# Optimization experiments

Hardware: AMD Instinct MI355X
Metric: run time of the kernel (lower is better)

## Reference

```python
import jax, jax.numpy as jnp
import numpy as np

U, B, S, R = 64, 256, 256, 512
N = 4096
EMA_DECAY = 0.99


def setup_inputs() -> dict:
    key = jax.random.key(0)
    ks = jax.random.split(key, 9)
    q_u = jax.random.uniform(ks[0], (N, U), dtype=jnp.float32)
    q_b = jax.random.uniform(ks[1], (N, B), dtype=jnp.float32)
    q_sigma = jax.random.normal(ks[2], (N, S), dtype=jnp.float32)
    delta_rule_target = jax.random.normal(ks[3], (N, R), dtype=jnp.float32)
    write_mask = jax.random.randint(ks[4], (N,), 0, 2).astype(bool)
    delta_rule_proto = 0.02 * jax.random.normal(ks[5], (U, B, R), dtype=jnp.float32)
    signature_proto = 0.02 * jax.random.normal(ks[6], (U, B, S), dtype=jnp.float32)
    ema_conf = jax.random.uniform(ks[7], (U, B), dtype=jnp.float32)
    usage_count = jnp.maximum(jax.random.uniform(ks[8], (U, B)) - 0.5, 0.0) * 100.0
    return {"q_u": q_u, "q_b": q_b, "q_sigma": q_sigma,
            "delta_rule_target": delta_rule_target, "write_mask": write_mask,
            "delta_rule_proto": delta_rule_proto, "signature_proto": signature_proto,
            "ema_conf": ema_conf, "usage_count": usage_count}


def _l2norm(x):
    return x / jnp.maximum(jnp.linalg.norm(x, axis=-1, keepdims=True), 1e-12)


def reference(q_u, q_b, q_sigma, delta_rule_target, write_mask,
              delta_rule_proto, signature_proto, ema_conf, usage_count):
    # ---------------- retrieve ----------------
    # joint attention over (operator, binding) cells; temperature == 1.0 branch
    joint = q_u[:, :, None] * q_b[:, None, :]                  # [N, U, B]
    valid = (usage_count > 0).astype(joint.dtype)              # [U, B]
    w = joint * valid
    denom = w.sum(axis=(-2, -1), keepdims=True)
    w = jnp.where(denom > 0, w / jnp.maximum(denom, 1e-6), jnp.zeros_like(w))
    memory_delta_rule = jnp.einsum('nub,ubr->nr', w, delta_rule_proto)
    memory_signature = jnp.einsum('nub,ubs->ns', w, signature_proto)
    base_conf = jnp.einsum('nub,ub->n', w, ema_conf)[:, None]  # [N, 1]
    cos = jnp.sum(_l2norm(q_sigma) * _l2norm(memory_signature + 1e-6),
                  axis=-1, keepdims=True)
    signature_agreement = 0.5 * (1.0 + cos)
    memory_conf = jnp.clip(base_conf * signature_agreement, 0.0, 1.0)

    # ---------------- update (vectorized scatter EMA) ----------------
    m = write_mask.astype(q_u.dtype)                           # [N]
    op_conf = q_u.max(axis=-1)
    op_id = jnp.argmax(q_u, axis=-1)
    bind_conf = q_b.max(axis=-1)
    bind_id = jnp.argmax(q_b, axis=-1)
    write_conf = op_conf * bind_conf                           # [N]
    cell = op_id * B + bind_id                                 # [N]
    num_cells = U * B
    wgt = write_conf * m
    sum_w = jax.ops.segment_sum(wgt, cell, num_segments=num_cells)          # [UB]
    sum_d = jax.ops.segment_sum(delta_rule_target * wgt[:, None], cell,
                                num_segments=num_cells)                     # [UB, R]
    sum_s = jax.ops.segment_sum(q_sigma * wgt[:, None], cell,
                                num_segments=num_cells)                     # [UB, S]
    cnt = jax.ops.segment_sum(m, cell, num_segments=num_cells)              # [UB]
    conf_sum = jnp.maximum(sum_w, 1e-6)
    delta_mean = (sum_d / conf_sum[:, None]).reshape(U, B, R)
    sigma_mean = (sum_s / conf_sum[:, None]).reshape(U, B, S)
    conf_mean = (sum_w / jnp.maximum(cnt, 1.0)).reshape(U, B)
    upd = (cnt > 0).reshape(U, B)
    new_delta_proto = jnp.where(upd[:, :, None],
                                EMA_DECAY * delta_rule_proto + (1.0 - EMA_DECAY) * delta_mean,
                                delta_rule_proto)
    new_signature_proto = jnp.where(upd[:, :, None],
                                    EMA_DECAY * signature_proto + (1.0 - EMA_DECAY) * sigma_mean,
                                    signature_proto)
    new_ema_conf = jnp.where(upd,
                             EMA_DECAY * ema_conf + (1.0 - EMA_DECAY) * conf_mean,
                             ema_conf)
    new_usage = usage_count + cnt.reshape(U, B)

    # ---------------- usage stats ----------------
    write_rate = m.mean()
    usage_fraction = (new_usage > 0).astype(jnp.float32).mean()
    dist = new_usage.reshape(-1)
    dist = dist / jnp.maximum(dist.sum(), 1e-6)
    usage_entropy = -(dist * jnp.log(dist + 1e-6)).sum() / np.log(max(2, num_cells))

    return (memory_delta_rule, memory_signature, memory_conf,
            new_delta_proto, new_signature_proto, new_ema_conf, new_usage,
            write_rate, usage_fraction, usage_entropy)
```

## Files before the change

kernel.cpp:

```cpp
#include <hip/hip_runtime.h>
#include <hip/hip_fp8.h>
#include <math.h>

#define NR 4096
#define UD 64
#define BD 256
#define SD 256
#define RD 512
#define UBD 16384
#define DECAY 0.99f

typedef unsigned char u8;
typedef __attribute__((ext_vector_type(4))) float f32x4;
typedef __attribute__((ext_vector_type(2))) long longx2;

#define OFF_MDR   0ull
#define OFF_MSIG  2097152ull
#define OFF_MCONF 3145728ull
#define OFF_NDP   3149824ull
#define OFF_NSP   11538432ull
#define OFF_NEC   15732736ull
#define OFF_NUS   15749120ull
#define OFF_SCAL  15765504ull

static __device__ __forceinline__ u8 f2e4m3(float x) {
  __hip_fp8_e4m3 h(x);
  return (u8)h.__x;
}

static __device__ __forceinline__ void gll16(const void* g, void* l) {
  __builtin_amdgcn_global_load_lds(
      (const __attribute__((address_space(1))) unsigned int*)g,
      (__attribute__((address_space(3))) unsigned int*)l, 16, 0, 0);
}

static __device__ __forceinline__ int perm64(int x) {
  return (((x >> 3) & 3) << 4) | (((x >> 5) & 1) << 3) | (x & 7);
}

__global__ __launch_bounds__(256) void prep_all_kernel(
    const float* __restrict__ q_u, const float* __restrict__ q_b,
    const float* __restrict__ q_sigma_unused,
    const float* __restrict__ dproto, const float* __restrict__ sproto,
    const float* __restrict__ usage, const float* __restrict__ ema,
    const unsigned char* __restrict__ wm,
    u8* __restrict__ qb8, float* __restrict__ quT, u8* __restrict__ PT8,
    float* __restrict__ denom, float* __restrict__ base_raw,
    float* __restrict__ wgt, int* __restrict__ cellid, float* __restrict__ mrow,
    float* __restrict__ sum_w, float* __restrict__ cnt)
{
  __shared__ __attribute__((aligned(16))) u8 sbuf[53248];
  __shared__ int s_flag;
  const int b = blockIdx.x;
  const int tid = threadIdx.x;

  if (b < 1024) {
    const int i = b * 256 + tid;
    const int idx = i * 4;
    const int row = idx >> 8;
    const int bb  = idx & 255;
    const float4 v = *(const float4*)(q_b + (size_t)idx);
    u8 tmp[4] = { f2e4m3(v.x), f2e4m3(v.y), f2e4m3(v.z), f2e4m3(v.w) };
    unsigned int wv; __builtin_memcpy(&wv, tmp, 4);
    const int nb = (bb & ~63) | perm64(bb & 63);
    *(unsigned int*)(qb8 + (size_t)row * BD + nb) = wv;
    return;
  }
  if (b < 1088) {
    float (*s)[65] = (float(*)[65])sbuf;
    const int n0 = (b - 1024) * 64;
    #pragma unroll
    for (int i = 0; i < 16; ++i) {
      const int idx = tid + i * 256;
      const int r = idx >> 6, u = idx & 63;
      s[r][u] = q_u[(size_t)(n0 + r) * UD + u];
    }
    __syncthreads();
    #pragma unroll
    for (int i = 0; i < 16; ++i) {
      const int idx = tid + i * 256;
      const int u = idx >> 6, r = idx & 63;
      quT[(size_t)u * NR + n0 + r] = s[r][u];
    }
    return;
  }
  if (b < 4160) {
    u8 (*s)[68] = (u8(*)[68])sbuf;
    const int idx = b - 1088;
    const int k0 = (idx & 255) * 64;
    const int rblk = idx >> 8;
    const float* src; int ld; int c0s;
    if (rblk < 8) { src = dproto; ld = RD; c0s = rblk * 64; }
    else          { src = sproto; ld = SD; c0s = (rblk - 8) * 64; }
    const int kl = tid >> 4;
    const int rl = (tid & 15) * 4;
    #pragma unroll
    for (int i = 0; i < 4; ++i) {
      const int k = kl + i * 16;
      const bool valid = usage[k0 + k] > 0.f;
      const float4 v = *(const float4*)(src + (size_t)(k0 + k) * ld + c0s + rl);
      s[k][rl + 0] = valid ? f2e4m3(v.x) : (u8)0;
      s[k][rl + 1] = valid ? f2e4m3(v.y) : (u8)0;
      s[k][rl + 2] = valid ? f2e4m3(v.z) : (u8)0;
      s[k][rl + 3] = valid ? f2e4m3(v.w) : (u8)0;
    }
    __syncthreads();
    const int rl2 = tid >> 4;
    const int kl2 = (tid & 15) * 4;
    #pragma unroll
    for (int i = 0; i < 4; ++i) {
      const int r = rl2 + i * 16;
      u8 tmp[4] = { s[kl2 + 0][r], s[kl2 + 1][r], s[kl2 + 2][r], s[kl2 + 3][r] };
      unsigned int wv; __builtin_memcpy(&wv, tmp, 4);
      *(unsigned int*)(PT8 + (size_t)(rblk * 64 + r) * UBD + k0 + perm64(kl2)) = wv;
    }
    return;
  }
  {
    float (*s_qu)[64]   = (float(*)[64])sbuf;
    float (*s_qbv)[256] = (float(*)[256])(sbuf + 4096);
    float (*s_pd)[256]  = (float(*)[256])(sbuf + 20480);
    float (*s_pc)[256]  = (float(*)[256])(sbuf + 36864);
    const int r0 = (b - 4160) * 16;
    {
      const float4 v = *(const float4*)(q_u + (size_t)r0 * UD + tid * 4);
      float* dst = &s_qu[0][0] + tid * 4;
      dst[0] = v.x; dst[1] = v.y; dst[2] = v.z; dst[3] = v.w;
    }
    {
      const float4* src = (const float4*)(q_b + (size_t)r0 * BD);
      float4* dst = (float4*)&s_qbv[0][0];
      #pragma unroll
      for (int i = 0; i < 4; ++i) dst[tid + i * 256] = src[tid + i * 256];
    }
    if (tid == 0) {
      const int*   wi = (const int*)wm;
      const float* wf = (const float*)wm;
      bool is_i32 = true, is_f32 = true;
      #pragma unroll
      for (int i = 0; i < 16; ++i) {
        int v = wi[i];
        if (v != 0 && v != 1) is_i32 = false;
        float f = wf[i];
        if (f != 0.f && f != 1.f) is_f32 = false;
      }
      s_flag = is_i32 ? 2 : (is_f32 ? 1 : 0);
    }
    __syncthreads();
    float accd[16], accc[16];
    #pragma unroll
    for (int r = 0; r < 16; ++r) { accd[r] = 0.f; accc[r] = 0.f; }
    #pragma unroll 2
    for (int u = 0; u < UD; ++u) {
      const float us = usage[u * BD + tid];
      const float em = ema[u * BD + tid];
      const float vm = (us > 0.f) ? 1.f : 0.f;
      const float ev = em * vm;
      #pragma unroll
      for (int r = 0; r < 16; ++r) {
        accd[r] += s_qu[r][u] * vm;
        accc[r] += s_qu[r][u] * ev;
      }
    }
    #pragma unroll
    for (int r = 0; r < 16; ++r) {
      s_pd[r][tid] = accd[r] * s_qbv[r][tid];
      s_pc[r][tid] = accc[r] * s_qbv[r][tid];
    }
    __syncthreads();
    const int w = tid >> 6, l = tid & 63;
    #pragma unroll
    for (int rr = 0; rr < 4; ++rr) {
      const int row = w * 4 + rr;
      float dsum = s_pd[row][l] + s_pd[row][l + 64] + s_pd[row][l + 128] + s_pd[row][l + 192];
      float csum = s_pc[row][l] + s_pc[row][l + 64] + s_pc[row][l + 128] + s_pc[row][l + 192];
      #pragma unroll
      for (int m = 1; m < 64; m <<= 1) {
        dsum += __shfl_xor(dsum, m);
        csum += __shfl_xor(csum, m);
      }
      float bv_ = s_qbv[row][l]; int bi_ = l;
      #pragma unroll
      for (int k = 1; k < 4; ++k) {
        const float v2 = s_qbv[row][l + k * 64];
        if (v2 > bv_) { bv_ = v2; bi_ = l + k * 64; }
      }
      #pragma unroll
      for (int m = 1; m < 64; m <<= 1) {
        const float ov = __shfl_xor(bv_, m);
        const int   oi = __shfl_xor(bi_, m);
        if (ov > bv_ || (ov == bv_ && oi < bi_)) { bv_ = ov; bi_ = oi; }
      }
      float uv_ = s_qu[row][l]; int ui_ = l;
      #pragma unroll
      for (int m = 1; m < 64; m <<= 1) {
        const float ov = __shfl_xor(uv_, m);
        const int   oi = __shfl_xor(ui_, m);
        if (ov > uv_ || (ov == uv_ && oi < ui_)) { uv_ = ov; ui_ = oi; }
      }
      if (l == 0) {
        const int n = r0 + row;
        const int fm = s_flag;
        float m;
        if (fm == 2)      m = (((const int*)wm)[n]   != 0)   ? 1.f : 0.f;
        else if (fm == 1) m = (((const float*)wm)[n] != 0.f) ? 1.f : 0.f;
        else              m = (wm[n] != 0)   ? 1.f : 0.f;
        const float wv = uv_ * bv_ * m;
        const int cell = ui_ * BD + bi_;
        denom[n]    = dsum;
        base_raw[n] = csum;
        wgt[n]      = wv;
        cellid[n]   = cell;
        mrow[n]     = m;
        if (m != 0.f) {
          atomicAdd(&sum_w[cell], wv);
          atomicAdd(&cnt[cell], 1.f);
        }
      }
    }
  }
}

__global__ __launch_bounds__(256, 2) void mfma_gemm_kernel(
    const float* __restrict__ quT, const u8* __restrict__ qb8,
    const u8* __restrict__ PT8, float* __restrict__ out,
    int* __restrict__ tk, int* __restrict__ gf, int* __restrict__ claimed)
{
  __shared__ __attribute__((aligned(16))) u8 smB[4 * 2 * 4096];
  __shared__ __attribute__((aligned(16))) float squT[16 * 128];
  __shared__ int s_work;
  const int tid = threadIdx.x;
  const int wid = tid >> 6, lane = tid & 63;

  const int wr = (wid >> 1) * 64, wc = (wid & 1) * 64;
  const int fr = lane & 15, kg = lane >> 4;
  const int srow  = lane >> 2;
  const int sslot = (lane & 3) ^ ((srow >> 1) & 3);
  u8* myB = smB + wid * 8192;
  int boff[4];
  #pragma unroll
  for (int nn = 0; nn < 4; ++nn)
    boff[nn] = (nn * 16 + fr) * 64 + ((kg ^ ((fr >> 1) & 3)) << 4);

  for (;;) {
    if (tid == 0) {
      unsigned int xcc;
      asm volatile("s_getreg_b32 %0, hwreg(HW_REG_XCC_ID)" : "=s"(xcc));
      const int x = (int)(xcc & 7u);
      const int t = atomicAdd(&tk[x], 1);
      int w = -1;
      if (t < 96) {
        const int cand = x * 96 + t;
        if (atomicCAS(&claimed[cand], 0, 1) == 0) w = cand;
      }
      while (w < 0) {
        const int g = atomicAdd(gf, 1);
        if (g >= 768) { w = -2; break; }
        if (atomicCAS(&claimed[g], 0, 1) == 0) w = g;
      }
      s_work = w;
    }
    __syncthreads();
    const int w = s_work;
    if (w < 0) return;

    const int bx = w & 31;
    const int combo = w >> 5;
    const int by = combo >> 2;
    const int bz = combo & 3;
    const int n0 = bx * 128;
    const int kbeg = bz * (UBD / 4);
    const int ubase = bz * 16;
    const int c0 = by * 128;

    float* obase; int ldO; int cc0;
    if (by < 4) { obase = out + OFF_MDR;  ldO = RD; cc0 = by * 128; }
    else        { obase = out + OFF_MSIG; ldO = SD; cc0 = (by - 4) * 128; }

    longx2 afrag[4][4];
    {
      const u8* ga = qb8 + (size_t)(n0 + wr + fr) * BD + kg * 16;
      #pragma unroll
      for (int m = 0; m < 4; ++m)
        #pragma unroll
        for (int q = 0; q < 4; ++q)
          afrag[m][q] = *(const longx2*)(ga + (size_t)m * 16 * BD + q * 64);
    }

    #pragma unroll
    for (int i = 0; i < 2; ++i) {
      const int u = wid * 4 + i * 2 + (lane >> 5);
      const float* src = quT + (size_t)(ubase + u) * NR + n0 + (lane & 31) * 4;
      gll16(src, (u8*)squT + (wid * 4 + i * 2) * 512);
    }
    const u8* gB = PT8 + (size_t)(c0 + wc + srow) * UBD + kbeg + sslot * 16;
    #pragma unroll
    for (int c = 0; c < 2; ++c)
      #pragma unroll
      for (int j = 0; j < 4; ++j)
        gll16(gB + (size_t)(j * 16) * UBD + c * 64, myB + c * 4096 + j * 1024);
    __syncthreads();

    f32x4 accm[4][4], accu[4][4];
    #pragma unroll
    for (int m = 0; m < 4; ++m)
      #pragma unroll
      for (int nn = 0; nn < 4; ++nn)
        accm[m][nn] = (f32x4){0.f, 0.f, 0.f, 0.f};

    for (int uc = 0; uc < 16; ++uc) {
      #pragma unroll
      for (int p4 = 0; p4 < 4; ++p4) {
        const int ph = uc * 4 + p4;
        if (p4 == 3 && uc == 15) asm volatile("s_waitcnt vmcnt(0)" ::: "memory");
        else                     asm volatile("s_waitcnt vmcnt(4)" ::: "memory");
        const u8* sb = myB + (ph & 1) * 4096;
        longx2 bv[4];
        #pragma unroll
        for (int nn = 0; nn < 4; ++nn)
          bv[nn] = *(const longx2*)(sb + boff[nn]);
        asm volatile("s_waitcnt lgkmcnt(0)" ::: "memory");
        if (!(uc == 15 && p4 >= 2)) {
          const u8* gs = gB + (size_t)(ph + 2) * 64;
          #pragma unroll
          for (int j = 0; j < 4; ++j)
            gll16(gs + (size_t)(j * 16) * UBD, myB + (ph & 1) * 4096 + j * 1024);
        }
        #pragma unroll
        for (int m = 0; m < 4; ++m)
          #pragma unroll
          for (int nn = 0; nn < 4; ++nn) {
            if (p4 == 0)
              accu[m][nn] = __builtin_amdgcn_mfma_f32_16x16x32_fp8_fp8(
                  afrag[m][p4].x, bv[nn].x, (f32x4){0.f, 0.f, 0.f, 0.f}, 0, 0, 0);
            else
              accu[m][nn] = __builtin_amdgcn_mfma_f32_16x16x32_fp8_fp8(
                  afrag[m][p4].x, bv[nn].x, accu[m][nn], 0, 0, 0);
          }
        #pragma unroll
        for (int m = 0; m < 4; ++m)
          #pragma unroll
          for (int nn = 0; nn < 4; ++nn)
            accu[m][nn] = __builtin_amdgcn_mfma_f32_16x16x32_fp8_fp8(
                afrag[m][p4].y, bv[nn].y, accu[m][nn], 0, 0, 0);
        if (p4 == 3) {
          const float* qs = squT + uc * 128 + wr + kg * 4;
          #pragma unroll
          for (int m = 0; m < 4; ++m) {
            const f32x4 qv = *(const f32x4*)(qs + m * 16);
            #pragma unroll
            for (int nn = 0; nn < 4; ++nn)
              accm[m][nn] += qv * accu[m][nn];
          }
        }
      }
    }

    #pragma unroll
    for (int m = 0; m < 4; ++m) {
      #pragma unroll
      for (int nn = 0; nn < 4; ++nn) {
        const int c = cc0 + wc + nn * 16 + fr;
        #pragma unroll
        for (int j = 0; j < 4; ++j) {
          const int r = n0 + wr + m * 16 + kg * 4 + j;
          atomicAdd(obase + (size_t)r * ldO + c, accm[m][nn][j]);
        }
      }
    }
  }
}

__global__ __launch_bounds__(256) void post_all_kernel(
    const float* __restrict__ q_sigma, const float* __restrict__ denom,
    const float* __restrict__ base_raw,
    const float* __restrict__ dproto, const float* __restrict__ sproto,
    const float* __restrict__ ema, const float* __restrict__ usage,
    const float* __restrict__ sum_w, const float* __restrict__ cnt,
    float* __restrict__ out)
{
  __shared__ float r1[256], r2[256], r3[256];
  const int b = blockIdx.x;
  const int t = threadIdx.x;

  if (b < 4096) {
    const int n = b;
    const float d = denom[n];
    const float scale = (d > 0.f) ? (1.f / fmaxf(d, 1e-6f)) : 0.f;
    float* mdr = out + OFF_MDR + (size_t)n * RD;
    mdr[t]       *= scale;
    mdr[t + 256] *= scale;
    float* msig = out + OFF_MSIG + (size_t)n * SD;
    const float s = msig[t] * scale;
    msig[t] = s;
    const float a = q_sigma[(size_t)n * SD + t];
    const float bb = s + 1e-6f;
    r1[t] = a * a; r2[t] = bb * bb; r3[t] = a * bb;
    __syncthreads();
    for (int st = 128; st > 0; st >>= 1) {
      if (t < st) { r1[t] += r1[t + st]; r2[t] += r2[t + st]; r3[t] += r3[t + st]; }
      __syncthreads();
    }
    if (t == 0) {
      const float na = fmaxf(sqrtf(r1[0]), 1e-12f);
      const float nb = fmaxf(sqrtf(r2[0]), 1e-12f);
      const float cosv = r3[0] / (na * nb);
      const float agree = 0.5f * (1.f + cosv);
      const float base = (d > 0.f) ? base_raw[n] / fmaxf(d, 1e-6f) : 0.f;
      out[OFF_MCONF + n] = fminf(fmaxf(base * agree, 0.f), 1.f);
    }
    return;
  }
  if (b < 8192) {
    const size_t nd = (size_t)UBD * RD;
    const size_t total = nd + (size_t)UBD * SD;
    float* outd = out + OFF_NDP;
    float* outs = out + OFF_NSP;
    for (size_t i = (size_t)(b - 4096) * 256 + t; i < total;
         i += (size_t)4096 * 256) {
      if (i < nd) {
        const float p = dproto[i];
        outd[i] = (cnt[(int)(i >> 9)] > 0.f) ? DECAY * p : p;
      } else {
        const size_t j = i - nd;
        const float p = sproto[j];
        outs[j] = (cnt[(int)(j >> 8)] > 0.f) ? DECAY * p : p;
      }
    }
    return;
  }
  if (b < 8256) {
    const int i = (b - 8192) * 256 + t;
    const float c = cnt[i];
    const float cm = sum_w[i] / fmaxf(c, 1.f);
    out[OFF_NEC + i] = (c > 0.f) ? DECAY * ema[i] + (1.f - DECAY) * cm : ema[i];
    out[OFF_NUS + i] = usage[i] + c;
    return;
  }
  {
    float scnt = 0.f, snz = 0.f, sus = 0.f;
    for (int i = t; i < UBD; i += 256) {
      const float c = cnt[i]; scnt += c;
      const float u = usage[i] + c;
      if (u > 0.f) snz += 1.f;
      sus += u;
    }
    r1[t] = scnt; r2[t] = snz; r3[t] = sus;
    __syncthreads();
    for (int s = 128; s > 0; s >>= 1) {
      if (t < s) { r1[t] += r1[t + s]; r2[t] += r2[t + s]; r3[t] += r3[t + s]; }
      __syncthreads();
    }
    const float total_cnt = r1[0], total_nz = r2[0], total_us = r3[0];
    __syncthreads();
    const float S = fmaxf(total_us, 1e-6f);
    float ent = 0.f;
    for (int i = t; i < UBD; i += 256) {
      const float d = (usage[i] + cnt[i]) / S;
      ent += d * logf(d + 1e-6f);
    }
    r1[t] = ent;
    __syncthreads();
    for (int s = 128; s > 0; s >>= 1) {
      if (t < s) { r1[t] += r1[t + s]; }
      __syncthreads();
    }
    if (t == 0) {
      out[OFF_SCAL + 0] = total_cnt / (float)NR;
      out[OFF_SCAL + 1] = total_nz / (float)UBD;
      out[OFF_SCAL + 2] = -r1[0] / 9.70406053f;
    }
  }
}

__global__ __launch_bounds__(256) void scatter2_kernel(
    const float* __restrict__ dtarget, const float* __restrict__ q_sigma,
    const float* __restrict__ wgt, const int* __restrict__ cellid,
    const float* __restrict__ mrow, const float* __restrict__ sum_w,
    float* __restrict__ outd, float* __restrict__ outs)
{
  const int n = blockIdx.x;
  if (mrow[n] == 0.f) return;
  const int t = threadIdx.x;
  const int c = cellid[n];
  const float cs = fmaxf(sum_w[c], 1e-6f);
  const float coef = (1.0f - DECAY) * wgt[n] / cs;
  atomicAdd(&outd[(size_t)c * RD + t],       dtarget[(size_t)n * RD + t] * coef);
  atomicAdd(&outd[(size_t)c * RD + t + 256], dtarget[(size_t)n * RD + t + 256] * coef);
  atomicAdd(&outs[(size_t)c * SD + t],       q_sigma[(size_t)n * SD + t] * coef);
}

extern "C" void kernel_launch(void* const* d_in, const int* in_sizes, int n_in,
                              void* d_out, int out_size, void* d_ws, size_t ws_size,
                              hipStream_t stream)
{
  const float* q_u    = (const float*)d_in[0];
  const float* q_b    = (const float*)d_in[1];
  const float* q_sig  = (const float*)d_in[2];
  const float* dtg    = (const float*)d_in[3];
  const unsigned char* wm = (const unsigned char*)d_in[4];
  const float* dproto = (const float*)d_in[5];
  const float* sproto = (const float*)d_in[6];
  const float* ema    = (const float*)d_in[7];
  const float* usage  = (const float*)d_in[8];
  float* out = (float*)d_out;

  float* wsf = (float*)d_ws;
  int*   wsi = (int*)d_ws;
  float* denom    = wsf + 16;
  float* base_raw = wsf + 16 + 4096;
  float* wgtb     = wsf + 16 + 8192;
  int*   cellid   = wsi + 16 + 12288;
  float* mrow     = wsf + 16 + 16384;
  float* sum_w    = wsf + 20496;
  float* cnt      = wsf + 20496 + 16384;
  int*   tk       = wsi + 53264;
  int*   gf       = wsi + 53272;
  int*   claimed  = wsi + 53280;

  u8*    PT8 = (u8*)(out + OFF_NDP);
  u8*    qb8 = PT8 + (size_t)768 * UBD;
  float* quT = (float*)(qb8 + (size_t)NR * BD);

  hipMemsetAsync(out, 0, (size_t)OFF_MCONF * sizeof(float), stream);
  hipMemsetAsync(sum_w, 0, (2u * UBD + 16 + 768) * sizeof(float), stream);

  prep_all_kernel<<<4416, 256, 0, stream>>>(q_u, q_b, q_sig, dproto, sproto,
                                            usage, ema, wm, qb8, quT, PT8,
                                            denom, base_raw, wgtb, cellid, mrow,
                                            sum_w, cnt);
  mfma_gemm_kernel<<<512, 256, 0, stream>>>(quT, qb8, PT8, out, tk, gf, claimed);
  post_all_kernel<<<8257, 256, 0, stream>>>(q_sig, denom, base_raw, dproto,
                                            sproto, ema, usage, sum_w, cnt, out);
  scatter2_kernel<<<NR, 256, 0, stream>>>(dtg, q_sig, wgtb, cellid, mrow, sum_w,
                                          out + OFF_NDP, out + OFF_NSP);
}
```

Measured before the change: 206.6 us.

## Fuse denominator scaling into GEMM epilogue and output zeroing into prep kernel

```diff
diff --git a/kernel.cpp b/kernel.cpp
--- a/kernel.cpp
+++ b/kernel.cpp
@@ -40,14 +40,14 @@
 
 __global__ __launch_bounds__(256) void prep_all_kernel(
     const float* __restrict__ q_u, const float* __restrict__ q_b,
-    const float* __restrict__ q_sigma_unused,
     const float* __restrict__ dproto, const float* __restrict__ sproto,
     const float* __restrict__ usage, const float* __restrict__ ema,
     const unsigned char* __restrict__ wm,
     u8* __restrict__ qb8, float* __restrict__ quT, u8* __restrict__ PT8,
     float* __restrict__ denom, float* __restrict__ base_raw,
     float* __restrict__ wgt, int* __restrict__ cellid, float* __restrict__ mrow,
-    float* __restrict__ sum_w, float* __restrict__ cnt)
+    float* __restrict__ sum_w, float* __restrict__ cnt,
+    float* __restrict__ out)
 {
   __shared__ __attribute__((aligned(16))) u8 sbuf[53248];
   __shared__ int s_flag;
@@ -114,6 +114,11 @@
       unsigned int wv; __builtin_memcpy(&wv, tmp, 4);
       *(unsigned int*)(PT8 + (size_t)(rblk * 64 + r) * UBD + k0 + perm64(kl2)) = wv;
     }
+    return;
+  }
+  if (b >= 4416) {
+    const size_t base = (size_t)(b - 4416) * 1024 + tid * 4;
+    *(float4*)(out + base) = (float4){0.f, 0.f, 0.f, 0.f};
     return;
   }
   {
@@ -223,7 +228,8 @@
 
 __global__ __launch_bounds__(256, 2) void mfma_gemm_kernel(
     const float* __restrict__ quT, const u8* __restrict__ qb8,
-    const u8* __restrict__ PT8, float* __restrict__ out,
+    const u8* __restrict__ PT8, const float* __restrict__ denom,
+    float* __restrict__ out,
     int* __restrict__ tk, int* __restrict__ gf, int* __restrict__ claimed)
 {
   __shared__ __attribute__((aligned(16))) u8 smB[4 * 2 * 4096];
@@ -336,13 +342,9 @@
             else
               accu[m][nn] = __builtin_amdgcn_mfma_f32_16x16x32_fp8_fp8(
                   afrag[m][p4].x, bv[nn].x, accu[m][nn], 0, 0, 0);
-          }
-        #pragma unroll
-        for (int m = 0; m < 4; ++m)
-          #pragma unroll
-          for (int nn = 0; nn < 4; ++nn)
             accu[m][nn] = __builtin_amdgcn_mfma_f32_16x16x32_fp8_fp8(
                 afrag[m][p4].y, bv[nn].y, accu[m][nn], 0, 0, 0);
+          }
         if (p4 == 3) {
           const float* qs = squT + uc * 128 + wr + kg * 4;
           #pragma unroll
@@ -356,6 +358,14 @@
       }
     }
 
+    float sc[4][4];
+    #pragma unroll
+    for (int m = 0; m < 4; ++m)
+      #pragma unroll
+      for (int j = 0; j < 4; ++j) {
+        const float d = denom[n0 + wr + m * 16 + kg * 4 + j];
+        sc[m][j] = (d > 0.f) ? (1.f / fmaxf(d, 1e-6f)) : 0.f;
+      }
     #pragma unroll
     for (int m = 0; m < 4; ++m) {
       #pragma unroll
@@ -364,7 +374,7 @@
         #pragma unroll
         for (int j = 0; j < 4; ++j) {
           const int r = n0 + wr + m * 16 + kg * 4 + j;
-          atomicAdd(obase + (size_t)r * ldO + c, accm[m][nn][j]);
+          atomicAdd(obase + (size_t)r * ldO + c, accm[m][nn][j] * sc[m][j]);
         }
       }
     }
@@ -385,16 +395,8 @@
 
   if (b < 4096) {
     const int n = b;
-    const float d = denom[n];
-    const float scale = (d > 0.f) ? (1.f / fmaxf(d, 1e-6f)) : 0.f;
-    float* mdr = out + OFF_MDR + (size_t)n * RD;
-    mdr[t]       *= scale;
-    mdr[t + 256] *= scale;
-    float* msig = out + OFF_MSIG + (size_t)n * SD;
-    const float s = msig[t] * scale;
-    msig[t] = s;
     const float a = q_sigma[(size_t)n * SD + t];
-    const float bb = s + 1e-6f;
+    const float bb = out[OFF_MSIG + (size_t)n * SD + t] + 1e-6f;
     r1[t] = a * a; r2[t] = bb * bb; r3[t] = a * bb;
     __syncthreads();
     for (int st = 128; st > 0; st >>= 1) {
@@ -406,6 +408,7 @@
       const float nb = fmaxf(sqrtf(r2[0]), 1e-12f);
       const float cosv = r3[0] / (na * nb);
       const float agree = 0.5f * (1.f + cosv);
+      const float d = denom[n];
       const float base = (d > 0.f) ? base_raw[n] / fmaxf(d, 1e-6f) : 0.f;
       out[OFF_MCONF + n] = fminf(fmaxf(base * agree, 0.f), 1.f);
     }
@@ -522,14 +525,14 @@
   u8*    qb8 = PT8 + (size_t)768 * UBD;
   float* quT = (float*)(qb8 + (size_t)NR * BD);
 
-  hipMemsetAsync(out, 0, (size_t)OFF_MCONF * sizeof(float), stream);
   hipMemsetAsync(sum_w, 0, (2u * UBD + 16 + 768) * sizeof(float), stream);
 
-  prep_all_kernel<<<4416, 256, 0, stream>>>(q_u, q_b, q_sig, dproto, sproto,
+  prep_all_kernel<<<7488, 256, 0, stream>>>(q_u, q_b, dproto, sproto,
                                             usage, ema, wm, qb8, quT, PT8,
                                             denom, base_raw, wgtb, cellid, mrow,
-                                            sum_w, cnt);
-  mfma_gemm_kernel<<<512, 256, 0, stream>>>(quT, qb8, PT8, out, tk, gf, claimed);
+                                            sum_w, cnt, out);
+  mfma_gemm_kernel<<<768, 256, 0, stream>>>(quT, qb8, PT8, denom, out,
+                                            tk, gf, claimed);
   post_all_kernel<<<8257, 256, 0, stream>>>(q_sig, denom, base_raw, dproto,
                                             sproto, ema, usage, sum_w, cnt, out);
   scatter2_kernel<<<NR, 256, 0, stream>>>(dtg, q_sig, wgtb, cellid, mrow, sum_w,
```

New measurement: 213.3 us. +3.3%, slower.
